# Kernel optimization log

Hardware: AMD Instinct MI355X
Metric: run time of the kernel (lower is better)

Reference implementation:

```python
import jax, jax.numpy as jnp
import numpy as np

BN_EPS = 1e-5

def _bn(h, gamma, beta, mean, var):
    # inference-mode BatchNorm1d
    return (h - mean) * jax.lax.rsqrt(var + BN_EPS) * gamma + beta


def setup_inputs() -> dict:
    key = jax.random.key(0)
    ks = jax.random.split(key, 16)
    N, E, D_in, D, L = 100000, 640000, 256, 128, 3
    s = 0.05
    return {
        "x": jax.random.normal(ks[0], (N, D_in), jnp.float32),
        "edge_index": jax.random.randint(ks[1], (2, E), 0, N, jnp.int32),
        "W_in": jax.random.normal(ks[2], (D_in, D), jnp.float32) * s,
        "b_in": jax.random.normal(ks[3], (D,), jnp.float32) * s,
        "bn_in_gamma": jax.random.uniform(ks[4], (D,), jnp.float32, 0.5, 1.5),
        "bn_in_beta": jax.random.normal(ks[5], (D,), jnp.float32) * s,
        "bn_in_mean": jax.random.normal(ks[6], (D,), jnp.float32) * s,
        "bn_in_var": jax.random.uniform(ks[7], (D,), jnp.float32, 0.5, 1.5),
        "Wl": jax.random.normal(ks[8], (L, D, D), jnp.float32) * s,
        "bl": jax.random.normal(ks[9], (L, D), jnp.float32) * s,
        "Wr": jax.random.normal(ks[10], (L, D, D), jnp.float32) * s,
        "bn_gamma": jax.random.uniform(ks[11], (L, D), jnp.float32, 0.5, 1.5),
        "bn_beta": jax.random.normal(ks[12], (L, D), jnp.float32) * s,
        "bn_mean": jax.random.normal(ks[13], (L, D), jnp.float32) * s,
        "bn_var": jax.random.uniform(ks[14], (L, D), jnp.float32, 0.5, 1.5),
    }


def reference(x, edge_index, W_in, b_in, bn_in_gamma, bn_in_beta, bn_in_mean,
              bn_in_var, Wl, bl, Wr, bn_gamma, bn_beta, bn_mean, bn_var):
    N = x.shape[0]
    src, dst = edge_index[0], edge_index[1]
    # in-degree (clamped to 1 so isolated nodes aggregate to 0, matching PyG mean)
    deg = jax.ops.segment_sum(jnp.ones_like(dst, jnp.float32), dst, num_segments=N)
    deg = jnp.maximum(deg, 1.0)[:, None]  # [N, 1]

    # input projection + BN + ReLU (dropout = identity in eval)
    h = jax.nn.relu(_bn(x @ W_in + b_in, bn_in_gamma, bn_in_beta, bn_in_mean, bn_in_var))

    L = Wl.shape[0]
    for l in range(L):
        # SAGEConv(mean): lin_l(mean_j h_j) + lin_r(h_i)
        agg = jax.ops.segment_sum(h[src], dst, num_segments=N) / deg  # [N, D]
        h_new = agg @ Wl[l] + bl[l] + h @ Wr[l]
        h_new = jax.nn.relu(_bn(h_new, bn_gamma[l], bn_beta[l], bn_mean[l], bn_var[l]))
        h = h + h_new  # residual
    return h
```

## Files before the change

### kernel.cpp

```cpp
#include <hip/hip_runtime.h>

#define BN_EPS 1e-5f

typedef __bf16 bf16x8 __attribute__((ext_vector_type(8)));
typedef float f32x4 __attribute__((ext_vector_type(4)));
typedef unsigned int uint;
typedef unsigned short ushort;

__device__ __forceinline__ ushort f2bf(float f) {
  union { float f; uint u; } v; v.f = f;
  uint r = v.u + 0x7FFF + ((v.u >> 16) & 1);
  return (ushort)(r >> 16);
}
__device__ __forceinline__ float bf2f_lo(uint u) {
  union { uint i; float f; } v; v.i = u << 16; return v.f;
}
__device__ __forceinline__ float bf2f_hi(uint u) {
  union { uint i; float f; } v; v.i = u & 0xffff0000u; return v.f;
}
__device__ __forceinline__ uint pack2(float a, float b) {
  return (uint)f2bf(a) | ((uint)f2bf(b) << 16);
}


__global__ void hist_kernel(const int* __restrict__ dst, int* __restrict__ cnt, int E) {
  int e = blockIdx.x * 256 + threadIdx.x;
  if (e < E) atomicAdd(&cnt[dst[e]], 1);
}

__global__ void reserve_prep_kernel(const int* __restrict__ cnt, int* __restrict__ rowbeg,
                                    int* __restrict__ cursor,
                                    const float* __restrict__ W_in, const float* __restrict__ Wl,
                                    const float* __restrict__ Wr, ushort* __restrict__ Bfm,
                                    int NB, int N) {
  int tid = threadIdx.x;
  int b = blockIdx.x;
  if (b >= NB) {
    int p = (b - NB) * 256 + tid;
    int mat = p >> 12;
    int rem = p & 4095;
    int half = rem >> 11;
    int rem2 = rem & 2047;
    int nt = rem2 >> 8, kt2 = (rem2 >> 6) & 3, lane = rem2 & 63;
    int n = nt * 16 + (lane & 15);
    int k0 = (half * 4 + kt2) * 32 + (lane >> 4) * 8;
    ushort tmp[8];
    #pragma unroll
    for (int j = 0; j < 8; ++j) {
      int k = k0 + j;
      float v;
      if (mat == 0) v = W_in[k * 128 + n];
      else {
        int l = mat - 1;
        v = (k < 128) ? Wl[l * 16384 + k * 128 + n] : Wr[l * 16384 + (k - 128) * 128 + n];
      }
      tmp[j] = f2bf(v);
    }
    *(uint4*)&Bfm[(size_t)p * 8] = *(const uint4*)tmp;
    return;
  }
  int i = b * 256 + tid;
  int v = (i < N) ? cnt[i] : 0;
  int lane = tid & 63;
  int x = v;
  #pragma unroll
  for (int off = 1; off < 64; off <<= 1) {
    int y = __shfl_up(x, off, 64);
    if (lane >= off) x += y;
  }
  int ret = 0;
  if (lane == 63) ret = atomicAdd(cursor, x);
  int base = __shfl(ret, 63);
  if (i < N) rowbeg[i] = base + x - v;
}

__global__ void fill_kernel(const int* __restrict__ src, const int* __restrict__ dst,
                            const int* __restrict__ rowbeg, int* __restrict__ cur,
                            int* __restrict__ col, int E) {
  int e = blockIdx.x * 256 + threadIdx.x;
  if (e < E) {
    int d = dst[e];
    int p = rowbeg[d] + atomicAdd(&cur[d], 1);
    col[p] = src[e];
  }
}


__global__ void agg_kernel(const int* __restrict__ rowbeg, const int* __restrict__ deg,
                           const int* __restrict__ col,
                           const ushort* __restrict__ h, ushort* __restrict__ agg, int N) {
  int node = blockIdx.x * 8 + (threadIdx.x >> 5);
  if (node >= N) return;
  int lane = threadIdx.x & 31;
  const ushort* hp = h + lane * 4;
  int beg = rowbeg[node];
  int d = deg[node];
  float di = 1.0f / (float)(d > 0 ? d : 1);
  float a0 = 0.f, a1 = 0.f, a2 = 0.f, a3 = 0.f;
  int e = beg, end = beg + d;
  for (; e + 3 < end; e += 4) {
    uint2 v0 = *(const uint2*)(hp + (size_t)col[e] * 128);
    uint2 v1 = *(const uint2*)(hp + (size_t)col[e + 1] * 128);
    uint2 v2 = *(const uint2*)(hp + (size_t)col[e + 2] * 128);
    uint2 v3 = *(const uint2*)(hp + (size_t)col[e + 3] * 128);
    a0 += (bf2f_lo(v0.x) + bf2f_lo(v1.x)) + (bf2f_lo(v2.x) + bf2f_lo(v3.x));
    a1 += (bf2f_hi(v0.x) + bf2f_hi(v1.x)) + (bf2f_hi(v2.x) + bf2f_hi(v3.x));
    a2 += (bf2f_lo(v0.y) + bf2f_lo(v1.y)) + (bf2f_lo(v2.y) + bf2f_lo(v3.y));
    a3 += (bf2f_hi(v0.y) + bf2f_hi(v1.y)) + (bf2f_hi(v2.y) + bf2f_hi(v3.y));
  }
  for (; e < end; ++e) {
    uint2 v0 = *(const uint2*)(hp + (size_t)col[e] * 128);
    a0 += bf2f_lo(v0.x); a1 += bf2f_hi(v0.x);
    a2 += bf2f_lo(v0.y); a3 += bf2f_hi(v0.y);
  }
  uint2 o;
  o.x = pack2(a0 * di, a1 * di);
  o.y = pack2(a2 * di, a3 * di);
  *(uint2*)(agg + (size_t)node * 128 + lane * 4) = o;
}


template<bool F32OUT>
__global__ __launch_bounds__(256, 4)
void gemm_layer(const ushort* __restrict__ A0, const ushort* __restrict__ A1,
                const ushort* __restrict__ Bfm, const float* __restrict__ bias,
                const float* __restrict__ gamma, const float* __restrict__ beta,
                const float* __restrict__ mean, const float* __restrict__ var,
                const ushort* __restrict__ residual, void* __restrict__ out, int N) {
  __shared__ float Cb_all[4 * 16 * 68];
  int tid = threadIdx.x, wave = tid >> 6, lane = tid & 63;
  int wm = wave >> 1, wn = wave & 1, quad = lane >> 4, l16 = lane & 15;
  int m0 = blockIdx.x * 64;

  int rowm[2];
  #pragma unroll
  for (int mt = 0; mt < 2; ++mt) {
    int r = m0 + wm * 32 + mt * 16 + l16;
    rowm[mt] = r < N ? r : N - 1;
  }

  uint4 a_buf[2][2], b_buf[2][4];
  #pragma unroll
  for (int mt = 0; mt < 2; ++mt)
    a_buf[0][mt] = *(const uint4*)(A0 + (size_t)rowm[mt] * 128 + quad * 8);
  {
    const ushort* bp = Bfm + (size_t)(wn * 4 * 256 + lane) * 8;
    #pragma unroll
    for (int nt = 0; nt < 4; ++nt)
      b_buf[0][nt] = *(const uint4*)(bp + nt * 2048);
  }

  f32x4 acc[2][4] = {};

  #pragma unroll
  for (int kt = 0; kt < 8; ++kt) {
    if (kt < 7) {
      int k1 = kt + 1;
      const ushort* bse = (k1 < 4) ? A0 : A1;
      int ko = (k1 & 3) * 32 + quad * 8;
      #pragma unroll
      for (int mt = 0; mt < 2; ++mt)
        a_buf[k1 & 1][mt] = *(const uint4*)(bse + (size_t)rowm[mt] * 128 + ko);
      const ushort* bp = Bfm + ((size_t)(k1 >> 2) * 16384 +
                                (size_t)((wn * 4) * 256 + (k1 & 3) * 64 + lane) * 8);
      #pragma unroll
      for (int nt = 0; nt < 4; ++nt)
        b_buf[k1 & 1][nt] = *(const uint4*)(bp + nt * 2048);
    }
    __builtin_amdgcn_sched_barrier(0);
    #pragma unroll
    for (int mt = 0; mt < 2; ++mt) {
      bf16x8 af = __builtin_bit_cast(bf16x8, a_buf[kt & 1][mt]);
      #pragma unroll
      for (int nt = 0; nt < 4; ++nt)
        acc[mt][nt] = __builtin_amdgcn_mfma_f32_16x16x32_bf16(
            af, __builtin_bit_cast(bf16x8, b_buf[kt & 1][nt]), acc[mt][nt], 0, 0, 0);
    }
  }

  #pragma unroll
  for (int nt = 0; nt < 4; ++nt) {
    int c = wn * 64 + nt * 16 + l16;
    float sc = gamma[c] * rsqrtf(var[c] + BN_EPS);
    float sh = beta[c] - mean[c] * sc;
    float bi = bias[c];
    #pragma unroll
    for (int mt = 0; mt < 2; ++mt)
      #pragma unroll
      for (int r = 0; r < 4; ++r)
        acc[mt][nt][r] = fmaxf((acc[mt][nt][r] + bi) * sc + sh, 0.f);
  }

  float* Cb = Cb_all + wave * (16 * 68);
  #pragma unroll
  for (int mt = 0; mt < 2; ++mt) {
    #pragma unroll
    for (int nt = 0; nt < 4; ++nt)
      #pragma unroll
      for (int r = 0; r < 4; ++r)
        Cb[(quad * 4 + r) * 68 + nt * 16 + l16] = acc[mt][nt][r];
    #pragma unroll
    for (int i = 0; i < 4; ++i) {
      int idx = i * 64 + lane, rowl = idx >> 4, seg = idx & 15;
      int grow = m0 + wm * 32 + mt * 16 + rowl;
      if (grow < N) {
        float4 vv = *(float4*)&Cb[rowl * 68 + seg * 4];
        uint2 rv = *(const uint2*)(residual + (size_t)grow * 128 + wn * 64 + seg * 4);
        vv.x += bf2f_lo(rv.x); vv.y += bf2f_hi(rv.x);
        vv.z += bf2f_lo(rv.y); vv.w += bf2f_hi(rv.y);
        if (F32OUT) {
          *(float4*)((float*)out + (size_t)grow * 128 + wn * 64 + seg * 4) = vv;
        } else {
          uint2 o;
          o.x = pack2(vv.x, vv.y); o.y = pack2(vv.z, vv.w);
          *(uint2*)((ushort*)out + (size_t)grow * 128 + wn * 64 + seg * 4) = o;
        }
      }
    }
  }
}


__global__ __launch_bounds__(256, 4)
void gemm_in(const float* __restrict__ X, const ushort* __restrict__ Bfm,
             const float* __restrict__ bias,
             const float* __restrict__ gamma, const float* __restrict__ beta,
             const float* __restrict__ mean, const float* __restrict__ var,
             ushort* __restrict__ out, int N) {
  __shared__ float Cb_all[4 * 16 * 68];
  int tid = threadIdx.x, wave = tid >> 6, lane = tid & 63;
  int wm = wave >> 1, wn = wave & 1, quad = lane >> 4, l16 = lane & 15;
  int m0 = blockIdx.x * 64;

  int rowm[2];
  #pragma unroll
  for (int mt = 0; mt < 2; ++mt) {
    int r = m0 + wm * 32 + mt * 16 + l16;
    rowm[mt] = r < N ? r : N - 1;
  }

  float4 f_buf[2][2][2];
  uint4 b_buf[2][4];
  #pragma unroll
  for (int mt = 0; mt < 2; ++mt) {
    const float* p = X + (size_t)rowm[mt] * 256 + quad * 8;
    f_buf[0][mt][0] = *(const float4*)p;
    f_buf[0][mt][1] = *(const float4*)(p + 4);
  }
  {
    const ushort* bp = Bfm + (size_t)(wn * 4 * 256 + lane) * 8;
    #pragma unroll
    for (int nt = 0; nt < 4; ++nt)
      b_buf[0][nt] = *(const uint4*)(bp + nt * 2048);
  }

  f32x4 acc[2][4] = {};

  #pragma unroll
  for (int kt = 0; kt < 8; ++kt) {
    if (kt < 7) {
      int k1 = kt + 1;
      int ko = k1 * 32 + quad * 8;
      #pragma unroll
      for (int mt = 0; mt < 2; ++mt) {
        const float* p = X + (size_t)rowm[mt] * 256 + ko;
        f_buf[k1 & 1][mt][0] = *(const float4*)p;
        f_buf[k1 & 1][mt][1] = *(const float4*)(p + 4);
      }
      const ushort* bp = Bfm + ((size_t)(k1 >> 2) * 16384 +
                                (size_t)((wn * 4) * 256 + (k1 & 3) * 64 + lane) * 8);
      #pragma unroll
      for (int nt = 0; nt < 4; ++nt)
        b_buf[k1 & 1][nt] = *(const uint4*)(bp + nt * 2048);
    }
    __builtin_amdgcn_sched_barrier(0);
    #pragma unroll
    for (int mt = 0; mt < 2; ++mt) {
      float4 lo = f_buf[kt & 1][mt][0], hi = f_buf[kt & 1][mt][1];
      uint4 av;
      av.x = pack2(lo.x, lo.y); av.y = pack2(lo.z, lo.w);
      av.z = pack2(hi.x, hi.y); av.w = pack2(hi.z, hi.w);
      bf16x8 af = __builtin_bit_cast(bf16x8, av);
      #pragma unroll
      for (int nt = 0; nt < 4; ++nt)
        acc[mt][nt] = __builtin_amdgcn_mfma_f32_16x16x32_bf16(
            af, __builtin_bit_cast(bf16x8, b_buf[kt & 1][nt]), acc[mt][nt], 0, 0, 0);
    }
  }

  #pragma unroll
  for (int nt = 0; nt < 4; ++nt) {
    int c = wn * 64 + nt * 16 + l16;
    float sc = gamma[c] * rsqrtf(var[c] + BN_EPS);
    float sh = beta[c] - mean[c] * sc;
    float bi = bias[c];
    #pragma unroll
    for (int mt = 0; mt < 2; ++mt)
      #pragma unroll
      for (int r = 0; r < 4; ++r)
        acc[mt][nt][r] = fmaxf((acc[mt][nt][r] + bi) * sc + sh, 0.f);
  }

  float* Cb = Cb_all + wave * (16 * 68);
  #pragma unroll
  for (int mt = 0; mt < 2; ++mt) {
    #pragma unroll
    for (int nt = 0; nt < 4; ++nt)
      #pragma unroll
      for (int r = 0; r < 4; ++r)
        Cb[(quad * 4 + r) * 68 + nt * 16 + l16] = acc[mt][nt][r];
    #pragma unroll
    for (int i = 0; i < 4; ++i) {
      int idx = i * 64 + lane, rowl = idx >> 4, seg = idx & 15;
      int grow = m0 + wm * 32 + mt * 16 + rowl;
      if (grow < N) {
        float4 vv = *(float4*)&Cb[rowl * 68 + seg * 4];
        uint2 o;
        o.x = pack2(vv.x, vv.y); o.y = pack2(vv.z, vv.w);
        *(uint2*)(out + (size_t)grow * 128 + wn * 64 + seg * 4) = o;
      }
    }
  }
}


extern "C" void kernel_launch(void* const* d_in, const int* in_sizes, int n_in,
                              void* d_out, int out_size, void* d_ws, size_t ws_size,
                              hipStream_t stream) {
  const float* x      = (const float*)d_in[0];
  const int*   eidx   = (const int*)d_in[1];
  const float* W_in   = (const float*)d_in[2];
  const float* b_in   = (const float*)d_in[3];
  const float* bng_in = (const float*)d_in[4];
  const float* bnb_in = (const float*)d_in[5];
  const float* bnm_in = (const float*)d_in[6];
  const float* bnv_in = (const float*)d_in[7];
  const float* Wl     = (const float*)d_in[8];
  const float* bl     = (const float*)d_in[9];
  const float* Wr     = (const float*)d_in[10];
  const float* bng    = (const float*)d_in[11];
  const float* bnb    = (const float*)d_in[12];
  const float* bnm    = (const float*)d_in[13];
  const float* bnv    = (const float*)d_in[14];

  const int N = in_sizes[0] / 256;
  const int E = in_sizes[1] / 2;
  const int NB = (N + 255) / 256;
  const int* src = eidx;
  const int* dst = eidx + E;

  char* ws = (char*)d_ws;
  size_t off = 0;
  auto alloc = [&](size_t bytes) {
    void* p = ws + off;
    off = (off + bytes + 255) & ~(size_t)255;
    return p;
  };
  int* zreg     = (int*)alloc((size_t)(2 * N + 1) * 4);
  int* cnt      = zreg;
  int* cur      = zreg + N;
  int* cursor   = zreg + 2 * N;
  int* rowbeg   = (int*)alloc((size_t)N * 4);
  int* col      = (int*)alloc((size_t)E * 4);
  ushort* Bfm   = (ushort*)alloc(4 * 32768 * 2);
  ushort* hA    = (ushort*)alloc((size_t)N * 128 * 2);
  ushort* hB    = (ushort*)alloc((size_t)N * 128 * 2);
  ushort* agg   = (ushort*)alloc((size_t)N * 128 * 2);
  (void)ws_size; (void)n_in; (void)out_size;

  const int EB = (E + 255) / 256;
  const int GB = (N + 63) / 64;

  hipMemsetAsync(zreg, 0, (size_t)(2 * N + 1) * 4, stream);
  hist_kernel<<<EB, 256, 0, stream>>>(dst, cnt, E);
  reserve_prep_kernel<<<NB + 64, 256, 0, stream>>>(cnt, rowbeg, cursor,
                                                   W_in, Wl, Wr, Bfm, NB, N);
  fill_kernel<<<EB, 256, 0, stream>>>(src, dst, rowbeg, cur, col, E);

  gemm_in<<<GB, 256, 0, stream>>>(x, Bfm, b_in, bng_in, bnb_in, bnm_in, bnv_in, hA, N);

  ushort* hbuf[2] = { hA, hB };
  for (int l = 0; l < 3; ++l) {
    const ushort* h_in = hbuf[l & 1];
    agg_kernel<<<(N + 7) / 8, 256, 0, stream>>>(rowbeg, cnt, col, h_in, agg, N);
    const ushort* BfmL = Bfm + (size_t)(l + 1) * 32768;
    const float* biasL = bl + l * 128;
    if (l < 2) {
      gemm_layer<false><<<GB, 256, 0, stream>>>(agg, h_in, BfmL, biasL,
          bng + l * 128, bnb + l * 128, bnm + l * 128, bnv + l * 128,
          h_in, (void*)hbuf[(l + 1) & 1], N);
    } else {
      gemm_layer<true><<<GB, 256, 0, stream>>>(agg, h_in, BfmL, biasL,
          bng + l * 128, bnb + l * 128, bnm + l * 128, bnv + l * 128,
          h_in, d_out, N);
    }
  }
}
```

Baseline: 468.0 us.

## Fuse all stages into one persistent cooperative kernel with grid syncs

Replaces the sequence of separate launches (memset, histogram, scan, fill, input GEMM, and per-layer aggregation and GEMM) with a single cooperative persistent kernel. Stages are separated by grid.sync, and blocks loop over tiles. The input GEMM now runs alongside the degree histogram in the same phase. This removes per-launch overhead and inter-kernel gaps. In exchange, occupancy is capped at a fixed persistent grid, grid-wide barriers are added, and register pressure from the merged code may lower the number of resident blocks.

Result: slower. 1.267 ms (+170.7%).

```diff
diff --git a/kernel.cpp b/kernel.cpp
--- a/kernel.cpp
+++ b/kernel.cpp
@@ -1,4 +1,7 @@
 #include <hip/hip_runtime.h>
+#include <hip/hip_cooperative_groups.h>
+
+namespace cg = cooperative_groups;
 
 #define BN_EPS 1e-5f
 
@@ -22,82 +25,230 @@
   return (uint)f2bf(a) | ((uint)f2bf(b) << 16);
 }
 
-
-__global__ void hist_kernel(const int* __restrict__ dst, int* __restrict__ cnt, int E) {
-  int e = blockIdx.x * 256 + threadIdx.x;
-  if (e < E) atomicAdd(&cnt[dst[e]], 1);
-}
-
-__global__ void reserve_prep_kernel(const int* __restrict__ cnt, int* __restrict__ rowbeg,
-                                    int* __restrict__ cursor,
-                                    const float* __restrict__ W_in, const float* __restrict__ Wl,
-                                    const float* __restrict__ Wr, ushort* __restrict__ Bfm,
-                                    int NB, int N) {
-  int tid = threadIdx.x;
-  int b = blockIdx.x;
-  if (b >= NB) {
-    int p = (b - NB) * 256 + tid;
-    int mat = p >> 12;
-    int rem = p & 4095;
-    int half = rem >> 11;
-    int rem2 = rem & 2047;
-    int nt = rem2 >> 8, kt2 = (rem2 >> 6) & 3, lane = rem2 & 63;
-    int n = nt * 16 + (lane & 15);
-    int k0 = (half * 4 + kt2) * 32 + (lane >> 4) * 8;
-    ushort tmp[8];
-    #pragma unroll
-    for (int j = 0; j < 8; ++j) {
-      int k = k0 + j;
-      float v;
-      if (mat == 0) v = W_in[k * 128 + n];
-      else {
-        int l = mat - 1;
-        v = (k < 128) ? Wl[l * 16384 + k * 128 + n] : Wr[l * 16384 + (k - 128) * 128 + n];
+struct Args {
+  const float* x;
+  const int* src;
+  const int* dst;
+  const float* W_in; const float* b_in;
+  const float* bng_in; const float* bnb_in; const float* bnm_in; const float* bnv_in;
+  const float* Wl; const float* bl; const float* Wr;
+  const float* bng; const float* bnb; const float* bnm; const float* bnv;
+  int* cnt; int* cur; int* cursor;
+  int* rowbeg; int* col;
+  ushort* Bfm; ushort* hA; ushort* hB; ushort* agg;
+  float* out;
+  int N, E, NB, EB, GB, NG;
+};
+
+__device__ __forceinline__ void gemm_in_tile(const Args& a, int t, float* Cb_all) {
+  int tid = threadIdx.x, wave = tid >> 6, lane = tid & 63;
+  int wm = wave >> 1, wn = wave & 1, quad = lane >> 4, l16 = lane & 15;
+  int m0 = t * 64;
+  const float* X = a.x;
+  int N = a.N;
+
+  int rowm[2];
+  #pragma unroll
+  for (int mt = 0; mt < 2; ++mt) {
+    int r = m0 + wm * 32 + mt * 16 + l16;
+    rowm[mt] = r < N ? r : N - 1;
+  }
+
+  float4 f_buf[2][2][2];
+  uint4 b_buf[2][4];
+  #pragma unroll
+  for (int mt = 0; mt < 2; ++mt) {
+    const float* p = X + (size_t)rowm[mt] * 256 + quad * 8;
+    f_buf[0][mt][0] = *(const float4*)p;
+    f_buf[0][mt][1] = *(const float4*)(p + 4);
+  }
+  {
+    const ushort* bp = a.Bfm + (size_t)(wn * 4 * 256 + lane) * 8;
+    #pragma unroll
+    for (int nt = 0; nt < 4; ++nt)
+      b_buf[0][nt] = *(const uint4*)(bp + nt * 2048);
+  }
+
+  f32x4 acc[2][4] = {};
+
+  #pragma unroll
+  for (int kt = 0; kt < 8; ++kt) {
+    if (kt < 7) {
+      int k1 = kt + 1;
+      int ko = k1 * 32 + quad * 8;
+      #pragma unroll
+      for (int mt = 0; mt < 2; ++mt) {
+        const float* p = X + (size_t)rowm[mt] * 256 + ko;
+        f_buf[k1 & 1][mt][0] = *(const float4*)p;
+        f_buf[k1 & 1][mt][1] = *(const float4*)(p + 4);
       }
-      tmp[j] = f2bf(v);
-    }
-    *(uint4*)&Bfm[(size_t)p * 8] = *(const uint4*)tmp;
-    return;
-  }
-  int i = b * 256 + tid;
-  int v = (i < N) ? cnt[i] : 0;
-  int lane = tid & 63;
-  int x = v;
-  #pragma unroll
-  for (int off = 1; off < 64; off <<= 1) {
-    int y = __shfl_up(x, off, 64);
-    if (lane >= off) x += y;
-  }
-  int ret = 0;
-  if (lane == 63) ret = atomicAdd(cursor, x);
-  int base = __shfl(ret, 63);
-  if (i < N) rowbeg[i] = base + x - v;
-}
-
-__global__ void fill_kernel(const int* __restrict__ src, const int* __restrict__ dst,
-                            const int* __restrict__ rowbeg, int* __restrict__ cur,
-                            int* __restrict__ col, int E) {
-  int e = blockIdx.x * 256 + threadIdx.x;
-  if (e < E) {
-    int d = dst[e];
-    int p = rowbeg[d] + atomicAdd(&cur[d], 1);
-    col[p] = src[e];
-  }
-}
-
-
-__global__ void agg_kernel(const int* __restrict__ rowbeg, const int* __restrict__ deg,
-                           const int* __restrict__ col,
-                           const ushort* __restrict__ h, ushort* __restrict__ agg, int N) {
-  int node = blockIdx.x * 8 + (threadIdx.x >> 5);
-  if (node >= N) return;
+      const ushort* bp = a.Bfm + ((size_t)(k1 >> 2) * 16384 +
+                                  (size_t)((wn * 4) * 256 + (k1 & 3) * 64 + lane) * 8);
+      #pragma unroll
+      for (int nt = 0; nt < 4; ++nt)
+        b_buf[k1 & 1][nt] = *(const uint4*)(bp + nt * 2048);
+    }
+    __builtin_amdgcn_sched_barrier(0);
+    #pragma unroll
+    for (int mt = 0; mt < 2; ++mt) {
+      float4 lo = f_buf[kt & 1][mt][0], hi = f_buf[kt & 1][mt][1];
+      uint4 av;
+      av.x = pack2(lo.x, lo.y); av.y = pack2(lo.z, lo.w);
+      av.z = pack2(hi.x, hi.y); av.w = pack2(hi.z, hi.w);
+      bf16x8 af = __builtin_bit_cast(bf16x8, av);
+      #pragma unroll
+      for (int nt = 0; nt < 4; ++nt)
+        acc[mt][nt] = __builtin_amdgcn_mfma_f32_16x16x32_bf16(
+            af, __builtin_bit_cast(bf16x8, b_buf[kt & 1][nt]), acc[mt][nt], 0, 0, 0);
+    }
+  }
+
+  #pragma unroll
+  for (int nt = 0; nt < 4; ++nt) {
+    int c = wn * 64 + nt * 16 + l16;
+    float sc = a.bng_in[c] * rsqrtf(a.bnv_in[c] + BN_EPS);
+    float sh = a.bnb_in[c] - a.bnm_in[c] * sc;
+    float bi = a.b_in[c];
+    #pragma unroll
+    for (int mt = 0; mt < 2; ++mt)
+      #pragma unroll
+      for (int r = 0; r < 4; ++r)
+        acc[mt][nt][r] = fmaxf((acc[mt][nt][r] + bi) * sc + sh, 0.f);
+  }
+
+  float* Cb = Cb_all + wave * (16 * 68);
+  #pragma unroll
+  for (int mt = 0; mt < 2; ++mt) {
+    #pragma unroll
+    for (int nt = 0; nt < 4; ++nt)
+      #pragma unroll
+      for (int r = 0; r < 4; ++r)
+        Cb[(quad * 4 + r) * 68 + nt * 16 + l16] = acc[mt][nt][r];
+    #pragma unroll
+    for (int i = 0; i < 4; ++i) {
+      int idx = i * 64 + lane, rowl = idx >> 4, seg = idx & 15;
+      int grow = m0 + wm * 32 + mt * 16 + rowl;
+      if (grow < N) {
+        float4 vv = *(float4*)&Cb[rowl * 68 + seg * 4];
+        uint2 o;
+        o.x = pack2(vv.x, vv.y); o.y = pack2(vv.z, vv.w);
+        *(uint2*)(a.hA + (size_t)grow * 128 + wn * 64 + seg * 4) = o;
+      }
+    }
+  }
+}
+
+__device__ __forceinline__ void gemm_layer_tile(const Args& a, int t, const ushort* h_in,
+                                                const ushort* BfmL, const float* biasL,
+                                                const float* gamma, const float* beta,
+                                                const float* mean, const float* var,
+                                                void* outp, bool f32out, float* Cb_all) {
+  int tid = threadIdx.x, wave = tid >> 6, lane = tid & 63;
+  int wm = wave >> 1, wn = wave & 1, quad = lane >> 4, l16 = lane & 15;
+  int m0 = t * 64;
+  int N = a.N;
+  const ushort* A0 = a.agg;
+  const ushort* A1 = h_in;
+
+  int rowm[2];
+  #pragma unroll
+  for (int mt = 0; mt < 2; ++mt) {
+    int r = m0 + wm * 32 + mt * 16 + l16;
+    rowm[mt] = r < N ? r : N - 1;
+  }
+
+  uint4 a_buf[2][2], b_buf[2][4];
+  #pragma unroll
+  for (int mt = 0; mt < 2; ++mt)
+    a_buf[0][mt] = *(const uint4*)(A0 + (size_t)rowm[mt] * 128 + quad * 8);
+  {
+    const ushort* bp = BfmL + (size_t)(wn * 4 * 256 + lane) * 8;
+    #pragma unroll
+    for (int nt = 0; nt < 4; ++nt)
+      b_buf[0][nt] = *(const uint4*)(bp + nt * 2048);
+  }
+
+  f32x4 acc[2][4] = {};
+
+  #pragma unroll
+  for (int kt = 0; kt < 8; ++kt) {
+    if (kt < 7) {
+      int k1 = kt + 1;
+      const ushort* bse = (k1 < 4) ? A0 : A1;
+      int ko = (k1 & 3) * 32 + quad * 8;
+      #pragma unroll
+      for (int mt = 0; mt < 2; ++mt)
+        a_buf[k1 & 1][mt] = *(const uint4*)(bse + (size_t)rowm[mt] * 128 + ko);
+      const ushort* bp = BfmL + ((size_t)(k1 >> 2) * 16384 +
+                                 (size_t)((wn * 4) * 256 + (k1 & 3) * 64 + lane) * 8);
+      #pragma unroll
+      for (int nt = 0; nt < 4; ++nt)
+        b_buf[k1 & 1][nt] = *(const uint4*)(bp + nt * 2048);
+    }
+    __builtin_amdgcn_sched_barrier(0);
+    #pragma unroll
+    for (int mt = 0; mt < 2; ++mt) {
+      bf16x8 af = __builtin_bit_cast(bf16x8, a_buf[kt & 1][mt]);
+      #pragma unroll
+      for (int nt = 0; nt < 4; ++nt)
+        acc[mt][nt] = __builtin_amdgcn_mfma_f32_16x16x32_bf16(
+            af, __builtin_bit_cast(bf16x8, b_buf[kt & 1][nt]), acc[mt][nt], 0, 0, 0);
+    }
+  }
+
+  #pragma unroll
+  for (int nt = 0; nt < 4; ++nt) {
+    int c = wn * 64 + nt * 16 + l16;
+    float sc = gamma[c] * rsqrtf(var[c] + BN_EPS);
+    float sh = beta[c] - mean[c] * sc;
+    float bi = biasL[c];
+    #pragma unroll
+    for (int mt = 0; mt < 2; ++mt)
+      #pragma unroll
+      for (int r = 0; r < 4; ++r)
+        acc[mt][nt][r] = fmaxf((acc[mt][nt][r] + bi) * sc + sh, 0.f);
+  }
+
+  float* Cb = Cb_all + wave * (16 * 68);
+  #pragma unroll
+  for (int mt = 0; mt < 2; ++mt) {
+    #pragma unroll
+    for (int nt = 0; nt < 4; ++nt)
+      #pragma unroll
+      for (int r = 0; r < 4; ++r)
+        Cb[(quad * 4 + r) * 68 + nt * 16 + l16] = acc[mt][nt][r];
+    #pragma unroll
+    for (int i = 0; i < 4; ++i) {
+      int idx = i * 64 + lane, rowl = idx >> 4, seg = idx & 15;
+      int grow = m0 + wm * 32 + mt * 16 + rowl;
+      if (grow < N) {
+        float4 vv = *(float4*)&Cb[rowl * 68 + seg * 4];
+        uint2 rv = *(const uint2*)(h_in + (size_t)grow * 128 + wn * 64 + seg * 4);
+        vv.x += bf2f_lo(rv.x); vv.y += bf2f_hi(rv.x);
+        vv.z += bf2f_lo(rv.y); vv.w += bf2f_hi(rv.y);
+        if (f32out) {
+          *(float4*)((float*)outp + (size_t)grow * 128 + wn * 64 + seg * 4) = vv;
+        } else {
+          uint2 o;
+          o.x = pack2(vv.x, vv.y); o.y = pack2(vv.z, vv.w);
+          *(uint2*)((ushort*)outp + (size_t)grow * 128 + wn * 64 + seg * 4) = o;
+        }
+      }
+    }
+  }
+}
+
+__device__ __forceinline__ void agg_group(const Args& a, int g, const ushort* h_in) {
+  int node = g * 8 + (threadIdx.x >> 5);
+  if (node >= a.N) return;
   int lane = threadIdx.x & 31;
-  const ushort* hp = h + lane * 4;
-  int beg = rowbeg[node];
-  int d = deg[node];
+  const ushort* hp = h_in + lane * 4;
+  int beg = a.rowbeg[node];
+  int d = a.cnt[node];
   float di = 1.0f / (float)(d > 0 ? d : 1);
   float a0 = 0.f, a1 = 0.f, a2 = 0.f, a3 = 0.f;
   int e = beg, end = beg + d;
+  const int* col = a.col;
   for (; e + 3 < end; e += 4) {
     uint2 v0 = *(const uint2*)(hp + (size_t)col[e] * 128);
     uint2 v1 = *(const uint2*)(hp + (size_t)col[e + 1] * 128);
@@ -116,210 +267,92 @@
   uint2 o;
   o.x = pack2(a0 * di, a1 * di);
   o.y = pack2(a2 * di, a3 * di);
-  *(uint2*)(agg + (size_t)node * 128 + lane * 4) = o;
-}
-
-
-template<bool F32OUT>
-__global__ __launch_bounds__(256, 4)
-void gemm_layer(const ushort* __restrict__ A0, const ushort* __restrict__ A1,
-                const ushort* __restrict__ Bfm, const float* __restrict__ bias,
-                const float* __restrict__ gamma, const float* __restrict__ beta,
-                const float* __restrict__ mean, const float* __restrict__ var,
-                const ushort* __restrict__ residual, void* __restrict__ out, int N) {
-  __shared__ float Cb_all[4 * 16 * 68];
-  int tid = threadIdx.x, wave = tid >> 6, lane = tid & 63;
-  int wm = wave >> 1, wn = wave & 1, quad = lane >> 4, l16 = lane & 15;
-  int m0 = blockIdx.x * 64;
-
-  int rowm[2];
-  #pragma unroll
-  for (int mt = 0; mt < 2; ++mt) {
-    int r = m0 + wm * 32 + mt * 16 + l16;
-    rowm[mt] = r < N ? r : N - 1;
-  }
-
-  uint4 a_buf[2][2], b_buf[2][4];
-  #pragma unroll
-  for (int mt = 0; mt < 2; ++mt)
-    a_buf[0][mt] = *(const uint4*)(A0 + (size_t)rowm[mt] * 128 + quad * 8);
-  {
-    const ushort* bp = Bfm + (size_t)(wn * 4 * 256 + lane) * 8;
-    #pragma unroll
-    for (int nt = 0; nt < 4; ++nt)
-      b_buf[0][nt] = *(const uint4*)(bp + nt * 2048);
-  }
-
-  f32x4 acc[2][4] = {};
-
-  #pragma unroll
-  for (int kt = 0; kt < 8; ++kt) {
-    if (kt < 7) {
-      int k1 = kt + 1;
-      const ushort* bse = (k1 < 4) ? A0 : A1;
-      int ko = (k1 & 3) * 32 + quad * 8;
-      #pragma unroll
-      for (int mt = 0; mt < 2; ++mt)
-        a_buf[k1 & 1][mt] = *(const uint4*)(bse + (size_t)rowm[mt] * 128 + ko);
-      const ushort* bp = Bfm + ((size_t)(k1 >> 2) * 16384 +
-                                (size_t)((wn * 4) * 256 + (k1 & 3) * 64 + lane) * 8);
-      #pragma unroll
-      for (int nt = 0; nt < 4; ++nt)
-        b_buf[k1 & 1][nt] = *(const uint4*)(bp + nt * 2048);
-    }
-    __builtin_amdgcn_sched_barrier(0);
-    #pragma unroll
-    for (int mt = 0; mt < 2; ++mt) {
-      bf16x8 af = __builtin_bit_cast(bf16x8, a_buf[kt & 1][mt]);
-      #pragma unroll
-      for (int nt = 0; nt < 4; ++nt)
-        acc[mt][nt] = __builtin_amdgcn_mfma_f32_16x16x32_bf16(
-            af, __builtin_bit_cast(bf16x8, b_buf[kt & 1][nt]), acc[mt][nt], 0, 0, 0);
-    }
-  }
-
-  #pragma unroll
-  for (int nt = 0; nt < 4; ++nt) {
-    int c = wn * 64 + nt * 16 + l16;
-    float sc = gamma[c] * rsqrtf(var[c] + BN_EPS);
-    float sh = beta[c] - mean[c] * sc;
-    float bi = bias[c];
-    #pragma unroll
-    for (int mt = 0; mt < 2; ++mt)
-      #pragma unroll
-      for (int r = 0; r < 4; ++r)
-        acc[mt][nt][r] = fmaxf((acc[mt][nt][r] + bi) * sc + sh, 0.f);
-  }
-
-  float* Cb = Cb_all + wave * (16 * 68);
-  #pragma unroll
-  for (int mt = 0; mt < 2; ++mt) {
-    #pragma unroll
-    for (int nt = 0; nt < 4; ++nt)
-      #pragma unroll
-      for (int r = 0; r < 4; ++r)
-        Cb[(quad * 4 + r) * 68 + nt * 16 + l16] = acc[mt][nt][r];
-    #pragma unroll
-    for (int i = 0; i < 4; ++i) {
-      int idx = i * 64 + lane, rowl = idx >> 4, seg = idx & 15;
-      int grow = m0 + wm * 32 + mt * 16 + rowl;
-      if (grow < N) {
-        float4 vv = *(float4*)&Cb[rowl * 68 + seg * 4];
-        uint2 rv = *(const uint2*)(residual + (size_t)grow * 128 + wn * 64 + seg * 4);
-        vv.x += bf2f_lo(rv.x); vv.y += bf2f_hi(rv.x);
-        vv.z += bf2f_lo(rv.y); vv.w += bf2f_hi(rv.y);
-        if (F32OUT) {
-          *(float4*)((float*)out + (size_t)grow * 128 + wn * 64 + seg * 4) = vv;
-        } else {
-          uint2 o;
-          o.x = pack2(vv.x, vv.y); o.y = pack2(vv.z, vv.w);
-          *(uint2*)((ushort*)out + (size_t)grow * 128 + wn * 64 + seg * 4) = o;
-        }
+  *(uint2*)(a.agg + (size_t)node * 128 + lane * 4) = o;
+}
+
+__global__ void mega(Args a) {
+  __shared__ __align__(16) float Cb_all[4 * 16 * 68];
+  cg::grid_group grid = cg::this_grid();
+  const int tid = threadIdx.x;
+  const int bid = blockIdx.x;
+  const int nblk = gridDim.x;
+  const int tstride = nblk * 256;
+  const int t0 = bid * 256 + tid;
+
+  for (int i = t0; i < 2 * a.N + 1; i += tstride) a.cnt[i] = 0;
+  for (int p = t0; p < 16384; p += tstride) {
+    int mat = p >> 12;
+    int rem = p & 4095;
+    int half = rem >> 11;
+    int rem2 = rem & 2047;
+    int nt = rem2 >> 8, kt2 = (rem2 >> 6) & 3, lane = rem2 & 63;
+    int n = nt * 16 + (lane & 15);
+    int k0 = (half * 4 + kt2) * 32 + (lane >> 4) * 8;
+    ushort tmp[8];
+    #pragma unroll
+    for (int j = 0; j < 8; ++j) {
+      int k = k0 + j;
+      float v;
+      if (mat == 0) v = a.W_in[k * 128 + n];
+      else {
+        int l = mat - 1;
+        v = (k < 128) ? a.Wl[l * 16384 + k * 128 + n]
+                      : a.Wr[l * 16384 + (k - 128) * 128 + n];
       }
-    }
-  }
-}
-
-
-__global__ __launch_bounds__(256, 4)
-void gemm_in(const float* __restrict__ X, const ushort* __restrict__ Bfm,
-             const float* __restrict__ bias,
-             const float* __restrict__ gamma, const float* __restrict__ beta,
-             const float* __restrict__ mean, const float* __restrict__ var,
-             ushort* __restrict__ out, int N) {
-  __shared__ float Cb_all[4 * 16 * 68];
-  int tid = threadIdx.x, wave = tid >> 6, lane = tid & 63;
-  int wm = wave >> 1, wn = wave & 1, quad = lane >> 4, l16 = lane & 15;
-  int m0 = blockIdx.x * 64;
-
-  int rowm[2];
-  #pragma unroll
-  for (int mt = 0; mt < 2; ++mt) {
-    int r = m0 + wm * 32 + mt * 16 + l16;
-    rowm[mt] = r < N ? r : N - 1;
-  }
-
-  float4 f_buf[2][2][2];
-  uint4 b_buf[2][4];
-  #pragma unroll
-  for (int mt = 0; mt < 2; ++mt) {
-    const float* p = X + (size_t)rowm[mt] * 256 + quad * 8;
-    f_buf[0][mt][0] = *(const float4*)p;
-    f_buf[0][mt][1] = *(const float4*)(p + 4);
-  }
-  {
-    const ushort* bp = Bfm + (size_t)(wn * 4 * 256 + lane) * 8;
-    #pragma unroll
-    for (int nt = 0; nt < 4; ++nt)
-      b_buf[0][nt] = *(const uint4*)(bp + nt * 2048);
-  }
-
-  f32x4 acc[2][4] = {};
-
-  #pragma unroll
-  for (int kt = 0; kt < 8; ++kt) {
-    if (kt < 7) {
-      int k1 = kt + 1;
-      int ko = k1 * 32 + quad * 8;
-      #pragma unroll
-      for (int mt = 0; mt < 2; ++mt) {
-        const float* p = X + (size_t)rowm[mt] * 256 + ko;
-        f_buf[k1 & 1][mt][0] = *(const float4*)p;
-        f_buf[k1 & 1][mt][1] = *(const float4*)(p + 4);
-      }
-      const ushort* bp = Bfm + ((size_t)(k1 >> 2) * 16384 +
-                                (size_t)((wn * 4) * 256 + (k1 & 3) * 64 + lane) * 8);
-      #pragma unroll
-      for (int nt = 0; nt < 4; ++nt)
-        b_buf[k1 & 1][nt] = *(const uint4*)(bp + nt * 2048);
-    }
-    __builtin_amdgcn_sched_barrier(0);
-    #pragma unroll
-    for (int mt = 0; mt < 2; ++mt) {
-      float4 lo = f_buf[kt & 1][mt][0], hi = f_buf[kt & 1][mt][1];
-      uint4 av;
-      av.x = pack2(lo.x, lo.y); av.y = pack2(lo.z, lo.w);
-      av.z = pack2(hi.x, hi.y); av.w = pack2(hi.z, hi.w);
-      bf16x8 af = __builtin_bit_cast(bf16x8, av);
-      #pragma unroll
-      for (int nt = 0; nt < 4; ++nt)
-        acc[mt][nt] = __builtin_amdgcn_mfma_f32_16x16x32_bf16(
-            af, __builtin_bit_cast(bf16x8, b_buf[kt & 1][nt]), acc[mt][nt], 0, 0, 0);
-    }
-  }
-
-  #pragma unroll
-  for (int nt = 0; nt < 4; ++nt) {
-    int c = wn * 64 + nt * 16 + l16;
-    float sc = gamma[c] * rsqrtf(var[c] + BN_EPS);
-    float sh = beta[c] - mean[c] * sc;
-    float bi = bias[c];
-    #pragma unroll
-    for (int mt = 0; mt < 2; ++mt)
-      #pragma unroll
-      for (int r = 0; r < 4; ++r)
-        acc[mt][nt][r] = fmaxf((acc[mt][nt][r] + bi) * sc + sh, 0.f);
-  }
-
-  float* Cb = Cb_all + wave * (16 * 68);
-  #pragma unroll
-  for (int mt = 0; mt < 2; ++mt) {
-    #pragma unroll
-    for (int nt = 0; nt < 4; ++nt)
-      #pragma unroll
-      for (int r = 0; r < 4; ++r)
-        Cb[(quad * 4 + r) * 68 + nt * 16 + l16] = acc[mt][nt][r];
-    #pragma unroll
-    for (int i = 0; i < 4; ++i) {
-      int idx = i * 64 + lane, rowl = idx >> 4, seg = idx & 15;
-      int grow = m0 + wm * 32 + mt * 16 + rowl;
-      if (grow < N) {
-        float4 vv = *(float4*)&Cb[rowl * 68 + seg * 4];
-        uint2 o;
-        o.x = pack2(vv.x, vv.y); o.y = pack2(vv.z, vv.w);
-        *(uint2*)(out + (size_t)grow * 128 + wn * 64 + seg * 4) = o;
-      }
-    }
+      tmp[j] = f2bf(v);
+    }
+    *(uint4*)&a.Bfm[(size_t)p * 8] = *(const uint4*)tmp;
+  }
+  grid.sync();
+
+  for (int vb = bid; vb < a.GB + a.EB; vb += nblk) {
+    if (vb < a.GB) {
+      gemm_in_tile(a, vb, Cb_all);
+    } else {
+      int e = (vb - a.GB) * 256 + tid;
+      if (e < a.E) atomicAdd(&a.cnt[a.dst[e]], 1);
+    }
+  }
+  grid.sync();
+
+  for (int vb = bid; vb < a.NB; vb += nblk) {
+    int i = vb * 256 + tid;
+    int v = (i < a.N) ? a.cnt[i] : 0;
+    int lane = tid & 63;
+    int x = v;
+    #pragma unroll
+    for (int off = 1; off < 64; off <<= 1) {
+      int y = __shfl_up(x, off, 64);
+      if (lane >= off) x += y;
+    }
+    int ret = 0;
+    if (lane == 63) ret = atomicAdd(a.cursor, x);
+    int base = __shfl(ret, 63);
+    if (i < a.N) a.rowbeg[i] = base + x - v;
+  }
+  grid.sync();
+
+  for (int e = t0; e < a.E; e += tstride) {
+    int d = a.dst[e];
+    int p = a.rowbeg[d] + atomicAdd(&a.cur[d], 1);
+    a.col[p] = a.src[e];
+  }
+  grid.sync();
+
+  #pragma unroll 1
+  for (int l = 0; l < 3; ++l) {
+    const ushort* h_in = (l & 1) ? a.hB : a.hA;
+    for (int g = bid; g < a.NG; g += nblk) agg_group(a, g, h_in);
+    grid.sync();
+    const ushort* BfmL = a.Bfm + (size_t)(l + 1) * 32768;
+    const float* biasL = a.bl + l * 128;
+    void* outp = (l == 0) ? (void*)a.hB : (l == 1) ? (void*)a.hA : (void*)a.out;
+    bool f32out = (l == 2);
+    for (int t = bid; t < a.GB; t += nblk)
+      gemm_layer_tile(a, t, h_in, BfmL, biasL,
+                      a.bng + l * 128, a.bnb + l * 128, a.bnm + l * 128, a.bnv + l * 128,
+                      outp, f32out, Cb_all);
+    if (l < 2) grid.sync();
   }
 }
 
@@ -327,27 +360,8 @@
 extern "C" void kernel_launch(void* const* d_in, const int* in_sizes, int n_in,
                               void* d_out, int out_size, void* d_ws, size_t ws_size,
                               hipStream_t stream) {
-  const float* x      = (const float*)d_in[0];
-  const int*   eidx   = (const int*)d_in[1];
-  const float* W_in   = (const float*)d_in[2];
-  const float* b_in   = (const float*)d_in[3];
-  const float* bng_in = (const float*)d_in[4];
-  const float* bnb_in = (const float*)d_in[5];
-  const float* bnm_in = (const float*)d_in[6];
-  const float* bnv_in = (const float*)d_in[7];
-  const float* Wl     = (const float*)d_in[8];
-  const float* bl     = (const float*)d_in[9];
-  const float* Wr     = (const float*)d_in[10];
-  const float* bng    = (const float*)d_in[11];
-  const float* bnb    = (const float*)d_in[12];
-  const float* bnm    = (const float*)d_in[13];
-  const float* bnv    = (const float*)d_in[14];
-
   const int N = in_sizes[0] / 256;
   const int E = in_sizes[1] / 2;
-  const int NB = (N + 255) / 256;
-  const int* src = eidx;
-  const int* dst = eidx + E;
 
   char* ws = (char*)d_ws;
   size_t off = 0;
@@ -357,9 +371,6 @@
     return p;
   };
   int* zreg     = (int*)alloc((size_t)(2 * N + 1) * 4);
-  int* cnt      = zreg;
-  int* cur      = zreg + N;
-  int* cursor   = zreg + 2 * N;
   int* rowbeg   = (int*)alloc((size_t)N * 4);
   int* col      = (int*)alloc((size_t)E * 4);
   ushort* Bfm   = (ushort*)alloc(4 * 32768 * 2);
@@ -368,31 +379,49 @@
   ushort* agg   = (ushort*)alloc((size_t)N * 128 * 2);
   (void)ws_size; (void)n_in; (void)out_size;
 
-  const int EB = (E + 255) / 256;
-  const int GB = (N + 63) / 64;
-
-  hipMemsetAsync(zreg, 0, (size_t)(2 * N + 1) * 4, stream);
-  hist_kernel<<<EB, 256, 0, stream>>>(dst, cnt, E);
-  reserve_prep_kernel<<<NB + 64, 256, 0, stream>>>(cnt, rowbeg, cursor,
-                                                   W_in, Wl, Wr, Bfm, NB, N);
-  fill_kernel<<<EB, 256, 0, stream>>>(src, dst, rowbeg, cur, col, E);
-
-  gemm_in<<<GB, 256, 0, stream>>>(x, Bfm, b_in, bng_in, bnb_in, bnm_in, bnv_in, hA, N);
-
-  ushort* hbuf[2] = { hA, hB };
-  for (int l = 0; l < 3; ++l) {
-    const ushort* h_in = hbuf[l & 1];
-    agg_kernel<<<(N + 7) / 8, 256, 0, stream>>>(rowbeg, cnt, col, h_in, agg, N);
-    const ushort* BfmL = Bfm + (size_t)(l + 1) * 32768;
-    const float* biasL = bl + l * 128;
-    if (l < 2) {
-      gemm_layer<false><<<GB, 256, 0, stream>>>(agg, h_in, BfmL, biasL,
-          bng + l * 128, bnb + l * 128, bnm + l * 128, bnv + l * 128,
-          h_in, (void*)hbuf[(l + 1) & 1], N);
-    } else {
-      gemm_layer<true><<<GB, 256, 0, stream>>>(agg, h_in, BfmL, biasL,
-          bng + l * 128, bnb + l * 128, bnm + l * 128, bnv + l * 128,
-          h_in, d_out, N);
-    }
-  }
-}
+  Args a;
+  a.x      = (const float*)d_in[0];
+  a.src    = (const int*)d_in[1];
+  a.dst    = (const int*)d_in[1] + E;
+  a.W_in   = (const float*)d_in[2];
+  a.b_in   = (const float*)d_in[3];
+  a.bng_in = (const float*)d_in[4];
+  a.bnb_in = (const float*)d_in[5];
+  a.bnm_in = (const float*)d_in[6];
+  a.bnv_in = (const float*)d_in[7];
+  a.Wl     = (const float*)d_in[8];
+  a.bl     = (const float*)d_in[9];
+  a.Wr     = (const float*)d_in[10];
+  a.bng    = (const float*)d_in[11];
+  a.bnb    = (const float*)d_in[12];
+  a.bnm    = (const float*)d_in[13];
+  a.bnv    = (const float*)d_in[14];
+  a.cnt    = zreg;
+  a.cur    = zreg + N;
+  a.cursor = zreg + 2 * N;
+  a.rowbeg = rowbeg;
+  a.col    = col;
+  a.Bfm    = Bfm;
+  a.hA     = hA;
+  a.hB     = hB;
+  a.agg    = agg;
+  a.out    = (float*)d_out;
+  a.N  = N;
+  a.E  = E;
+  a.NB = (N + 255) / 256;
+  a.EB = (E + 255) / 256;
+  a.GB = (N + 63) / 64;
+  a.NG = (N + 7) / 8;
+
+  static int s_grid = 0;
+  if (s_grid == 0) {
+    int nb = 0;
+    hipError_t err = hipOccupancyMaxActiveBlocksPerMultiprocessor(&nb, mega, 256, 0);
+    if (err != hipSuccess || nb < 1) nb = 2;
+    if (nb > 8) nb = 8;
+    s_grid = nb * 256;
+  }
+
+  void* kargs[] = { (void*)&a };
+  hipLaunchCooperativeKernel((const void*)mega, dim3(s_grid), dim3(256), kargs, 0, stream);
+}
```

## Fuse degree histogram into input GEMM launch and mask aggregation tail loop

Applied to the files above, without the earlier changes.

Weight preparation is split into its own small kernel, and the edge-degree histogram now runs as extra blocks of the input-projection GEMM launch, so the atomic histogram overlaps the dense GEMM. The reserve/prefix kernel and the CSR fill are moved after that launch. The aggregation loop drops its scalar remainder loop: every iteration issues four gathers, with out-of-range indices clamped and their values zeroed. This adds redundant loads for tail edges and mixes heterogeneous blocks in one launch.

After: 437.8 us. 1.07x faster.

```diff
diff --git a/kernel.cpp b/kernel.cpp
--- a/kernel.cpp
+++ b/kernel.cpp
@@ -23,43 +23,36 @@
 }
 
 
-__global__ void hist_kernel(const int* __restrict__ dst, int* __restrict__ cnt, int E) {
-  int e = blockIdx.x * 256 + threadIdx.x;
-  if (e < E) atomicAdd(&cnt[dst[e]], 1);
-}
-
-__global__ void reserve_prep_kernel(const int* __restrict__ cnt, int* __restrict__ rowbeg,
-                                    int* __restrict__ cursor,
-                                    const float* __restrict__ W_in, const float* __restrict__ Wl,
-                                    const float* __restrict__ Wr, ushort* __restrict__ Bfm,
-                                    int NB, int N) {
+__global__ void prep_weights_fm(const float* __restrict__ W_in, const float* __restrict__ Wl,
+                                const float* __restrict__ Wr, ushort* __restrict__ Bfm) {
+  int p = blockIdx.x * 256 + threadIdx.x;
+  int mat = p >> 12;
+  int rem = p & 4095;
+  int half = rem >> 11;
+  int rem2 = rem & 2047;
+  int nt = rem2 >> 8, kt2 = (rem2 >> 6) & 3, lane = rem2 & 63;
+  int n = nt * 16 + (lane & 15);
+  int k0 = (half * 4 + kt2) * 32 + (lane >> 4) * 8;
+  ushort tmp[8];
+  #pragma unroll
+  for (int j = 0; j < 8; ++j) {
+    int k = k0 + j;
+    float v;
+    if (mat == 0) v = W_in[k * 128 + n];
+    else {
+      int l = mat - 1;
+      v = (k < 128) ? Wl[l * 16384 + k * 128 + n] : Wr[l * 16384 + (k - 128) * 128 + n];
+    }
+    tmp[j] = f2bf(v);
+  }
+  *(uint4*)&Bfm[(size_t)p * 8] = *(const uint4*)tmp;
+}
+
+
+__global__ void reserve_kernel(const int* __restrict__ cnt, int* __restrict__ rowbeg,
+                               int* __restrict__ cursor, int N) {
   int tid = threadIdx.x;
-  int b = blockIdx.x;
-  if (b >= NB) {
-    int p = (b - NB) * 256 + tid;
-    int mat = p >> 12;
-    int rem = p & 4095;
-    int half = rem >> 11;
-    int rem2 = rem & 2047;
-    int nt = rem2 >> 8, kt2 = (rem2 >> 6) & 3, lane = rem2 & 63;
-    int n = nt * 16 + (lane & 15);
-    int k0 = (half * 4 + kt2) * 32 + (lane >> 4) * 8;
-    ushort tmp[8];
-    #pragma unroll
-    for (int j = 0; j < 8; ++j) {
-      int k = k0 + j;
-      float v;
-      if (mat == 0) v = W_in[k * 128 + n];
-      else {
-        int l = mat - 1;
-        v = (k < 128) ? Wl[l * 16384 + k * 128 + n] : Wr[l * 16384 + (k - 128) * 128 + n];
-      }
-      tmp[j] = f2bf(v);
-    }
-    *(uint4*)&Bfm[(size_t)p * 8] = *(const uint4*)tmp;
-    return;
-  }
-  int i = b * 256 + tid;
+  int i = blockIdx.x * 256 + tid;
   int v = (i < N) ? cnt[i] : 0;
   int lane = tid & 63;
   int x = v;
@@ -96,22 +89,26 @@
   int beg = rowbeg[node];
   int d = deg[node];
   float di = 1.0f / (float)(d > 0 ? d : 1);
+  int end = beg + d;
   float a0 = 0.f, a1 = 0.f, a2 = 0.f, a3 = 0.f;
-  int e = beg, end = beg + d;
-  for (; e + 3 < end; e += 4) {
-    uint2 v0 = *(const uint2*)(hp + (size_t)col[e] * 128);
-    uint2 v1 = *(const uint2*)(hp + (size_t)col[e + 1] * 128);
-    uint2 v2 = *(const uint2*)(hp + (size_t)col[e + 2] * 128);
-    uint2 v3 = *(const uint2*)(hp + (size_t)col[e + 3] * 128);
+  #pragma unroll 1
+  for (int e = beg; e < end; e += 4) {
+    int i1 = e + 1, i2 = e + 2, i3 = e + 3;
+    int c0 = col[e];
+    int c1 = col[i1 < end ? i1 : e];
+    int c2 = col[i2 < end ? i2 : e];
+    int c3 = col[i3 < end ? i3 : e];
+    uint2 v0 = *(const uint2*)(hp + (size_t)c0 * 128);
+    uint2 v1 = *(const uint2*)(hp + (size_t)c1 * 128);
+    uint2 v2 = *(const uint2*)(hp + (size_t)c2 * 128);
+    uint2 v3 = *(const uint2*)(hp + (size_t)c3 * 128);
+    if (i1 >= end) { v1.x = 0u; v1.y = 0u; }
+    if (i2 >= end) { v2.x = 0u; v2.y = 0u; }
+    if (i3 >= end) { v3.x = 0u; v3.y = 0u; }
     a0 += (bf2f_lo(v0.x) + bf2f_lo(v1.x)) + (bf2f_lo(v2.x) + bf2f_lo(v3.x));
     a1 += (bf2f_hi(v0.x) + bf2f_hi(v1.x)) + (bf2f_hi(v2.x) + bf2f_hi(v3.x));
     a2 += (bf2f_lo(v0.y) + bf2f_lo(v1.y)) + (bf2f_lo(v2.y) + bf2f_lo(v3.y));
     a3 += (bf2f_hi(v0.y) + bf2f_hi(v1.y)) + (bf2f_hi(v2.y) + bf2f_hi(v3.y));
-  }
-  for (; e < end; ++e) {
-    uint2 v0 = *(const uint2*)(hp + (size_t)col[e] * 128);
-    a0 += bf2f_lo(v0.x); a1 += bf2f_hi(v0.x);
-    a2 += bf2f_lo(v0.y); a3 += bf2f_hi(v0.y);
   }
   uint2 o;
   o.x = pack2(a0 * di, a1 * di);
@@ -222,12 +219,19 @@
 
 
 __global__ __launch_bounds__(256, 4)
-void gemm_in(const float* __restrict__ X, const ushort* __restrict__ Bfm,
-             const float* __restrict__ bias,
-             const float* __restrict__ gamma, const float* __restrict__ beta,
-             const float* __restrict__ mean, const float* __restrict__ var,
-             ushort* __restrict__ out, int N) {
+void gemm_in_hist(const float* __restrict__ X, const ushort* __restrict__ Bfm,
+                  const float* __restrict__ bias,
+                  const float* __restrict__ gamma, const float* __restrict__ beta,
+                  const float* __restrict__ mean, const float* __restrict__ var,
+                  ushort* __restrict__ out,
+                  const int* __restrict__ dst, int* __restrict__ cnt,
+                  int N, int E, int GB) {
   __shared__ float Cb_all[4 * 16 * 68];
+  if (blockIdx.x >= GB) {
+    int e = (blockIdx.x - GB) * 256 + threadIdx.x;
+    if (e < E) atomicAdd(&cnt[dst[e]], 1);
+    return;
+  }
   int tid = threadIdx.x, wave = tid >> 6, lane = tid & 63;
   int wm = wave >> 1, wn = wave & 1, quad = lane >> 4, l16 = lane & 15;
   int m0 = blockIdx.x * 64;
@@ -372,12 +376,13 @@
   const int GB = (N + 63) / 64;
 
   hipMemsetAsync(zreg, 0, (size_t)(2 * N + 1) * 4, stream);
-  hist_kernel<<<EB, 256, 0, stream>>>(dst, cnt, E);
-  reserve_prep_kernel<<<NB + 64, 256, 0, stream>>>(cnt, rowbeg, cursor,
-                                                   W_in, Wl, Wr, Bfm, NB, N);
+  prep_weights_fm<<<64, 256, 0, stream>>>(W_in, Wl, Wr, Bfm);
+
+  gemm_in_hist<<<GB + EB, 256, 0, stream>>>(x, Bfm, b_in, bng_in, bnb_in, bnm_in, bnv_in,
+                                            hA, dst, cnt, N, E, GB);
+
+  reserve_kernel<<<NB, 256, 0, stream>>>(cnt, rowbeg, cursor, N);
   fill_kernel<<<EB, 256, 0, stream>>>(src, dst, rowbeg, cur, col, E);
-
-  gemm_in<<<GB, 256, 0, stream>>>(x, Bfm, b_in, bng_in, bnb_in, bnm_in, bnv_in, hA, N);
 
   ushort* hbuf[2] = { hA, hB };
   for (int l = 0; l < 3; ++l) {
```
